# Performance work log

Measured on AMD Instinct MI355X. Metric: run time of the kernel, lower is better.

The kernel has to match this reference:

```python
import math
import jax, jax.numpy as jnp
import numpy as np

NUM_PRE_NMS = 2000
NMS_THR = 0.7
MIN_SIZE = 16.0
LOG_MAX = math.log(1000.0 / 16)  # clamp on dh, dw as in the torch module

B, A, H, W = 8, 3, 200, 304
STRIDE = 4


def _make_anchors():
    # grid anchors, channel-last anchor ordering to match permute(0,2,3,1)
    sizes = np.array([32.0, 64.0, 128.0], dtype=np.float32)  # A sizes
    ys = (np.arange(H, dtype=np.float32) + 0.5) * STRIDE
    xs = (np.arange(W, dtype=np.float32) + 0.5) * STRIDE
    cy, cx = np.meshgrid(ys, xs, indexing="ij")  # [H,W]
    cx = cx[:, :, None]
    cy = cy[:, :, None]
    half = (sizes / 2.0)[None, None, :]  # [1,1,A]
    anc = np.stack([cx - half, cy - half, cx + half, cy + half], axis=-1)  # [H,W,A,4]
    anc = anc.reshape(-1, 4)  # [H*W*A, 4]
    anc = np.broadcast_to(anc[None], (B, anc.shape[0], 4)).copy()
    return jnp.asarray(anc)


def setup_inputs() -> dict:
    key = jax.random.key(0)
    k1, k2 = jax.random.split(key)
    cls_logits = jax.random.normal(k1, (B, A, H, W), dtype=jnp.float32)
    regs = jax.random.normal(k2, (B, 4 * A, H, W), dtype=jnp.float32) * 0.1
    anchors = _make_anchors()
    return {"cls_logits": cls_logits, "regs": regs, "anchors": anchors,
            "image_h": 800, "image_w": 1216}


def _box_iou(boxes):
    # boxes: [K,4] -> iou [K,K]
    x1, y1, x2, y2 = boxes[:, 0], boxes[:, 1], boxes[:, 2], boxes[:, 3]
    area = (x2 - x1) * (y2 - y1)
    ix1 = jnp.maximum(x1[:, None], x1[None, :])
    iy1 = jnp.maximum(y1[:, None], y1[None, :])
    ix2 = jnp.minimum(x2[:, None], x2[None, :])
    iy2 = jnp.minimum(y2[:, None], y2[None, :])
    iw = jnp.clip(ix2 - ix1, 0.0)
    ih = jnp.clip(iy2 - iy1, 0.0)
    inter = iw * ih
    union = area[:, None] + area[None, :] - inter
    return inter / jnp.maximum(union, 1e-6)


def _nms_one(boxes, valid):
    # boxes sorted by descending score; greedy suppression, fixed-size keep mask
    k = boxes.shape[0]
    iou = _box_iou(boxes)
    later = jnp.arange(k)

    def body(i, keep):
        sup = (iou[i] > NMS_THR) & keep[i] & (later > i)
        return keep & ~sup

    return jax.lax.fori_loop(0, k, body, valid)


def reference(cls_logits, regs, anchors, image_h, image_w):
    b = cls_logits.shape[0]
    # scores/regs in channel-last anchor order (matches permute(0,2,3,1))
    scores = jnp.transpose(cls_logits, (0, 2, 3, 1)).reshape(b, -1)       # [B,N]
    deltas = jnp.transpose(regs, (0, 2, 3, 1)).reshape(b, -1, 4)          # [B,N,4]
    n = scores.shape[1]
    k = min(NUM_PRE_NMS, n)

    top_scores, idx = jax.lax.top_k(scores, k)                            # [B,K]
    top_deltas = jnp.take_along_axis(deltas, idx[:, :, None], axis=1)     # [B,K,4]
    top_anchors = jnp.take_along_axis(anchors, idx[:, :, None], axis=1)   # [B,K,4]

    dx, dy = top_deltas[..., 0], top_deltas[..., 1]
    dh = jnp.minimum(top_deltas[..., 2], LOG_MAX)
    dw = jnp.minimum(top_deltas[..., 3], LOG_MAX)
    ah = top_anchors[..., 3] - top_anchors[..., 1]
    aw = top_anchors[..., 2] - top_anchors[..., 0]
    cx = aw / 2
    cy = ah / 2
    px = cx + dx * aw
    py = cy + dy * ah
    ph = jnp.exp(dh) * ah
    pw = jnp.exp(dw) * aw
    boxes = jnp.stack([px - pw / 2, py - ph / 2, px + pw / 2, py + ph / 2], axis=-1)  # [B,K,4]

    # size filter on clamped coords (as in _nms)
    w_img = jnp.float32(image_w)
    h_img = jnp.float32(image_h)
    bw = jnp.clip(boxes[..., 2], 0.0, w_img) - jnp.clip(boxes[..., 0], 0.0, w_img)
    bh = jnp.clip(boxes[..., 3], 0.0, h_img) - jnp.clip(boxes[..., 1], 0.0, h_img)
    valid = (bw >= MIN_SIZE) & (bh >= MIN_SIZE)

    keep = jax.vmap(_nms_one)(boxes, valid)                               # [B,K]
    out_boxes = boxes * keep[..., None].astype(boxes.dtype)
    return out_boxes, top_scores, keep
```

## Files before the change

### kernel.cpp

```cpp
#include <hip/hip_runtime.h>

#define HWSZ 60800
#define NA 3
#define NTOT 182400
#define KSEL 2000
#define BUFCAP 2048
#define CANDCAP 8192
#define NBATCH 8
#define GSPLIT 128
#define LOG_MAX_F 4.135166556742356f

#define OFF_H1    0
#define OFF_CCNT  65536
#define ZR_BYTES  65568
#define OFF_SEL   65568
#define OFF_BOX   65696
#define OFF_VALID 321696
#define OFF_SUP   385696
#define OFF_CAND  385696

__device__ __forceinline__ unsigned int xform(float f) {
    unsigned int b = __float_as_uint(f);
    return b ^ ((unsigned int)((int)b >> 31) | 0x80000000u);
}

__global__ __launch_bounds__(256) void k_hist1(const float* __restrict__ cls,
                                               unsigned int* __restrict__ hist1) {
    int b = blockIdx.y, part = blockIdx.x, tid = threadIdx.x;
    __shared__ unsigned int h[2048];
    for (int i = tid; i < 2048; i += 256) h[i] = 0u;
    __syncthreads();
    const float4* base4 = (const float4*)(cls + (size_t)b * NTOT);
    const int n4 = NTOT / 4;
    int per = (n4 + GSPLIT - 1) / GSPLIT;
    int lo = part * per, hi = lo + per;
    if (hi > n4) hi = n4;
    for (int i = lo + tid; i < hi; i += 256) {
        float4 v = base4[i];
        atomicAdd(&h[xform(v.x) >> 21], 1u);
        atomicAdd(&h[xform(v.y) >> 21], 1u);
        atomicAdd(&h[xform(v.z) >> 21], 1u);
        atomicAdd(&h[xform(v.w) >> 21], 1u);
    }
    __syncthreads();
    unsigned int* gh = hist1 + b * 2048;
    for (int i = tid; i < 2048; i += 256)
        if (h[i]) atomicAdd(&gh[i], h[i]);
}

__global__ __launch_bounds__(1024) void k_scan1(const unsigned int* __restrict__ hist1,
                                                uint4* __restrict__ selinfo) {
    int b = blockIdx.x, tid = threadIdx.x;
    __shared__ unsigned int sa[2048], sb[2048];
    const unsigned int* h = hist1 + b * 2048;
    sa[tid] = h[tid];
    sa[tid + 1024] = h[tid + 1024];
    unsigned int* src = sa; unsigned int* dst = sb;
    for (int d = 1; d < 2048; d <<= 1) {
        __syncthreads();
        dst[tid] = src[tid] + ((tid + d < 2048) ? src[tid + d] : 0u);
        int i2 = tid + 1024;
        dst[i2] = src[i2] + ((i2 + d < 2048) ? src[i2 + d] : 0u);
        unsigned int* t = src; src = dst; dst = t;
    }
    __syncthreads();
    #pragma unroll
    for (int k = 0; k < 2; ++k) {
        int i = tid + k * 1024;
        unsigned int c = src[i];
        unsigned int cn = (i < 2047) ? src[i + 1] : 0u;
        if (c >= KSEL && cn < KSEL)
            selinfo[b] = make_uint4((unsigned int)i, cn, KSEL - cn, 0u);
    }
}

__global__ __launch_bounds__(256) void k_gather(const float* __restrict__ cls,
                                                const uint4* __restrict__ selinfo,
                                                unsigned long long* __restrict__ cand,
                                                unsigned int* __restrict__ ccnt) {
    int b = blockIdx.y, part = blockIdx.x, tid = threadIdx.x;
    unsigned int bin = selinfo[b].x;
    __shared__ unsigned long long lbuf[1024];
    __shared__ unsigned int lcnt, gbase;
    if (tid == 0) lcnt = 0u;
    __syncthreads();
    const float4* base4 = (const float4*)(cls + (size_t)b * NTOT);
    const int n4 = NTOT / 4;
    int per = (n4 + GSPLIT - 1) / GSPLIT;
    int lo = part * per, hi = lo + per;
    if (hi > n4) hi = n4;
    for (int i = lo + tid; i < hi; i += 256) {
        float4 v = base4[i];
        float vals[4] = {v.x, v.y, v.z, v.w};
        int idx0 = i * 4;
        #pragma unroll
        for (int q = 0; q < 4; ++q) {
            unsigned int u = xform(vals[q]);
            if ((u >> 21) >= bin) {
                int idx = idx0 + q;
                int a = idx / HWSZ;
                int hw = idx - a * HWSZ;
                unsigned int n = (unsigned int)(hw * NA + a);
                unsigned int pos = atomicAdd(&lcnt, 1u);
                if (pos < 1024u)
                    lbuf[pos] = ((unsigned long long)u << 32) | (unsigned long long)(~n);
            }
        }
    }
    __syncthreads();
    if (tid == 0) {
        unsigned int c = lcnt < 1024u ? lcnt : 1024u;
        gbase = atomicAdd(&ccnt[b], c);
    }
    __syncthreads();
    unsigned int c = lcnt < 1024u ? lcnt : 1024u;
    unsigned int gb = gbase;
    for (unsigned int i = tid; i < c; i += 256) {
        unsigned int p = gb + i;
        if (p < CANDCAP) cand[(size_t)b * CANDCAP + p] = lbuf[i];
    }
}

__global__ __launch_bounds__(1024) void k_sort_decode(
        const unsigned long long* __restrict__ cand,
        const unsigned int* __restrict__ ccnt,
        const uint4* __restrict__ selinfo,
        const float* __restrict__ regs,
        const float* __restrict__ anchors,
        const int* __restrict__ img_h,
        const int* __restrict__ img_w,
        float* __restrict__ out_scores,
        float4* __restrict__ boxes_ws,
        unsigned int* __restrict__ valid_ws) {
    int b = blockIdx.x;
    int tid = threadIdx.x;
    __shared__ unsigned long long arr[BUFCAP];
    __shared__ unsigned int sa[2048], sb[2048];
    __shared__ unsigned int acnt, shT;
    uint4 si = selinfo[b];
    unsigned int bin = si.x, krem = si.z;
    unsigned int m = ccnt[b];
    if (m > CANDCAP) m = CANDCAP;
    const unsigned long long* cb = cand + (size_t)b * CANDCAP;

    sa[tid] = 0u; sa[tid + 1024] = 0u;
    if (tid == 0) acnt = 0u;
    __syncthreads();
    for (unsigned int i = tid; i < m; i += 1024) {
        unsigned int u = (unsigned int)(cb[i] >> 32);
        if ((u >> 21) == bin) atomicAdd(&sa[(u >> 10) & 2047u], 1u);
    }
    unsigned int* src = sa; unsigned int* dst = sb;
    for (int d = 1; d < 2048; d <<= 1) {
        __syncthreads();
        dst[tid] = src[tid] + ((tid + d < 2048) ? src[tid + d] : 0u);
        int i2 = tid + 1024;
        dst[i2] = src[i2] + ((i2 + d < 2048) ? src[i2 + d] : 0u);
        unsigned int* t = src; src = dst; dst = t;
    }
    __syncthreads();
    #pragma unroll
    for (int k = 0; k < 2; ++k) {
        int i = tid + k * 1024;
        unsigned int c = src[i];
        unsigned int cn = (i < 2047) ? src[i + 1] : 0u;
        if (c >= krem && cn < krem)
            shT = (bin << 21) | ((unsigned int)i << 10);
    }
    __syncthreads();
    unsigned int T = shT;

    int lane = tid & 63;
    unsigned long long lmask = (1ULL << lane) - 1ULL;
    unsigned int mr = (m + 1023u) & ~1023u;
    for (unsigned int i = tid; i < mr; i += 1024) {
        bool pred = false;
        unsigned long long key = 0ULL;
        if (i < m) {
            key = cb[i];
            pred = ((unsigned int)(key >> 32)) >= T;
        }
        unsigned long long mask = __ballot(pred);
        unsigned int cw = (unsigned int)__popcll(mask);
        unsigned int base = 0u;
        if (lane == 0 && cw) base = atomicAdd(&acnt, cw);
        base = __shfl(base, 0, 64);
        if (pred) {
            unsigned int pos = base + (unsigned int)__popcll(mask & lmask);
            if (pos < BUFCAP) arr[pos] = key;
        }
    }
    __syncthreads();
    unsigned int total = acnt < BUFCAP ? acnt : BUFCAP;
    for (unsigned int i = tid; i < BUFCAP; i += 1024)
        if (i >= total) arr[i] = 0ULL;
    __syncthreads();

    for (int k = 2; k <= BUFCAP; k <<= 1) {
        for (int j = k >> 1; j > 0; j >>= 1) {
            for (int i = tid; i < BUFCAP; i += 1024) {
                int ixj = i ^ j;
                if (ixj > i) {
                    unsigned long long x = arr[i], y = arr[ixj];
                    bool up = (i & k) == 0;
                    if (up ? (x < y) : (x > y)) { arr[i] = y; arr[ixj] = x; }
                }
            }
            __syncthreads();
        }
    }

    int hv = img_h[0];
    int wv = img_w[0];
    float himg = (hv > 0 && hv < 100000) ? (float)hv : __int_as_float(hv);
    float wimg = (wv > 0 && wv < 100000) ? (float)wv : __int_as_float(wv);

    for (int r = tid; r < KSEL; r += 1024) {
        unsigned long long packed = arr[r];
        size_t o = (size_t)b * KSEL + r;
        if (packed == 0ULL) {
            out_scores[o] = 0.f;
            boxes_ws[o] = make_float4(0.f, 0.f, 0.f, 0.f);
            valid_ws[o] = 0u;
            continue;
        }
        unsigned int u = (unsigned int)(packed >> 32);
        unsigned int n = ~((unsigned int)packed);
        unsigned int bits = (u & 0x80000000u) ? (u & 0x7FFFFFFFu) : ~u;
        float score = __uint_as_float(bits);
        int a = (int)(n % NA);
        int hw = (int)(n / NA);
        const float* rp = regs + ((size_t)b * (4 * NA) + 4 * a) * HWSZ + hw;
        float dx = rp[0 * HWSZ];
        float dy = rp[1 * HWSZ];
        float dh = rp[2 * HWSZ];
        float dw = rp[3 * HWSZ];
        const float* ap = anchors + ((size_t)b * NTOT + n) * 4;
        float ax1 = ap[0], ay1 = ap[1], ax2 = ap[2], ay2 = ap[3];
        float ahh = ay2 - ay1;
        float aww = ax2 - ax1;
        float cx = aww * 0.5f;
        float cy = ahh * 0.5f;
        float px = cx + dx * aww;
        float py = cy + dy * ahh;
        dh = fminf(dh, LOG_MAX_F);
        dw = fminf(dw, LOG_MAX_F);
        float ph = expf(dh) * ahh;
        float pw = expf(dw) * aww;
        float x1 = px - pw * 0.5f;
        float y1 = py - ph * 0.5f;
        float x2 = px + pw * 0.5f;
        float y2 = py + ph * 0.5f;
        float bwv = fminf(fmaxf(x2, 0.f), wimg) - fminf(fmaxf(x1, 0.f), wimg);
        float bhv = fminf(fmaxf(y2, 0.f), himg) - fminf(fmaxf(y1, 0.f), himg);
        unsigned int valid = (bwv >= 16.f && bhv >= 16.f) ? 1u : 0u;
        out_scores[o] = score;
        boxes_ws[o] = make_float4(x1, y1, x2, y2);
        valid_ws[o] = valid;
    }
}

__global__ __launch_bounds__(256) void k_supmat(const float4* __restrict__ boxes_ws,
                                                unsigned long long* __restrict__ sup) {
    int ct = blockIdx.x;
    int rt = blockIdx.y;
    int b  = blockIdx.z;
    int tid = threadIdx.x;
    __shared__ float4 colbox[64];
    int j0 = ct * 64;
    if (tid < 64) {
        int jl = j0 + tid;
        colbox[tid] = (jl < KSEL) ? boxes_ws[(size_t)b * KSEL + jl]
                                  : make_float4(0.f, 0.f, 0.f, 0.f);
    }
    __syncthreads();
    int i = rt * 256 + tid;
    if (i >= KSEL) return;
    float4 bi = boxes_ws[(size_t)b * KSEL + i];
    float area_i = (bi.z - bi.x) * (bi.w - bi.y);
    unsigned long long word = 0ULL;
    #pragma unroll 8
    for (int jj = 0; jj < 64; ++jj) {
        int j = j0 + jj;
        float4 bj = colbox[jj];
        float area_j = (bj.z - bj.x) * (bj.w - bj.y);
        float ix1 = fmaxf(bi.x, bj.x);
        float iy1 = fmaxf(bi.y, bj.y);
        float ix2 = fminf(bi.z, bj.z);
        float iy2 = fminf(bi.w, bj.w);
        float iw = fmaxf(ix2 - ix1, 0.f);
        float ih = fmaxf(iy2 - iy1, 0.f);
        float inter = iw * ih;
        float uni = area_i + area_j - inter;
        float iou = inter / fmaxf(uni, 1e-6f);
        bool s = (j > i) && (j < KSEL) && (iou > 0.7f);
        if (s) word |= (1ULL << jj);
    }
    sup[((size_t)b * KSEL + i) * 32 + ct] = word;
}

__global__ __launch_bounds__(256) void k_nms_scan(const unsigned long long* __restrict__ sup,
                                                  const unsigned int* __restrict__ valid_ws,
                                                  const float4* __restrict__ boxes_ws,
                                                  float* __restrict__ out_boxes,
                                                  float* __restrict__ out_keep) {
    int b = blockIdx.x;
    int tid = threadIdx.x;
    int lane = tid & 63;
    int myword = tid & 31;
    __shared__ unsigned long long kws[32];
    __shared__ unsigned long long fin[32];
    __shared__ unsigned long long diag[64];
    __shared__ unsigned int accw[64];
    const unsigned long long* srow = sup + (size_t)b * KSEL * 32;

    if (tid < 32) {
        unsigned long long kw = 0ULL;
        const uint4* vv = (const uint4*)(valid_ws + (size_t)b * KSEL);
        #pragma unroll 4
        for (int q = 0; q < 16; ++q) {
            uint4 x = vv[tid * 16 + q];
            int base = q * 4;
            if (x.x) kw |= 1ULL << (base + 0);
            if (x.y) kw |= 1ULL << (base + 1);
            if (x.z) kw |= 1ULL << (base + 2);
            if (x.w) kw |= 1ULL << (base + 3);
        }
        if (tid == 31) kw &= 0xFFFFULL;
        kws[tid] = kw;
    }
    if (tid < 64) accw[tid] = 0u;

    unsigned long long curv[8], nxt[8];
    #pragma unroll
    for (int k = 0; k < 8; ++k) curv[k] = srow[tid + k * 256];

    for (int w = 0; w < 32; ++w) {
        if (myword == w) {
            #pragma unroll
            for (int k = 0; k < 8; ++k) diag[(tid >> 5) + k * 8] = curv[k];
        }
        __syncthreads();

        if (w < 31) {
            int gbase = (w + 1) * 2048;
            #pragma unroll
            for (int k = 0; k < 8; ++k) {
                int e = tid + k * 256;
                int row = (w + 1) * 64 + (e >> 5);
                nxt[k] = (row < KSEL) ? srow[gbase + e] : 0ULL;
            }
        }

        unsigned long long dval = diag[lane];
        unsigned int dlo = (unsigned int)dval;
        unsigned int dhi = (unsigned int)(dval >> 32);
        unsigned long long k0 = kws[w];
        unsigned long long pend = ((unsigned long long)accw[w * 2 + 1] << 32)
                                  | (unsigned long long)accw[w * 2];
        unsigned long long c64 = k0 & ~pend;
        unsigned int clo = __builtin_amdgcn_readfirstlane((unsigned int)c64);
        unsigned int chi = __builtin_amdgcn_readfirstlane((unsigned int)(c64 >> 32));
        unsigned long long cur = ((unsigned long long)chi << 32) | (unsigned long long)clo;
        #pragma unroll
        for (int bit = 0; bit < 64; ++bit) {
            if ((cur >> bit) & 1ULL) {
                unsigned int lo = (unsigned int)__builtin_amdgcn_readlane((int)dlo, bit);
                unsigned int hi = (unsigned int)__builtin_amdgcn_readlane((int)dhi, bit);
                cur &= ~(((unsigned long long)hi << 32) | (unsigned long long)lo);
            }
        }
        if (tid == 0) fin[w] = cur;

        unsigned long long v = 0ULL;
        #pragma unroll
        for (int k = 0; k < 8; ++k) {
            int row = (tid + k * 256) >> 5;
            if ((cur >> row) & 1ULL) v |= curv[k];
        }
        v |= __shfl_xor(v, 32, 64);
        if (lane < 32 && v) {
            atomicOr(&accw[myword * 2], (unsigned int)v);
            atomicOr(&accw[myword * 2 + 1], (unsigned int)(v >> 32));
        }

        #pragma unroll
        for (int k = 0; k < 8; ++k) curv[k] = nxt[k];
    }
    __syncthreads();

    for (int r = tid; r < KSEL; r += 256) {
        float kf = (float)((fin[r >> 6] >> (r & 63)) & 1ULL);
        size_t o = (size_t)b * KSEL + r;
        out_keep[o] = kf;
        float4 bx = boxes_ws[o];
        float* ob = out_boxes + o * 4;
        ob[0] = bx.x * kf;
        ob[1] = bx.y * kf;
        ob[2] = bx.z * kf;
        ob[3] = bx.w * kf;
    }
}

extern "C" void kernel_launch(void* const* d_in, const int* in_sizes, int n_in,
                              void* d_out, int out_size, void* d_ws, size_t ws_size,
                              hipStream_t stream) {
    const float* cls     = (const float*)d_in[0];
    const float* regs    = (const float*)d_in[1];
    const float* anchors = (const float*)d_in[2];
    const int*   img_h   = (const int*)d_in[3];
    const int*   img_w   = (const int*)d_in[4];

    float* out = (float*)d_out;
    float* out_boxes  = out;
    float* out_scores = out + 64000;
    float* out_keep   = out + 80000;

    char* ws = (char*)d_ws;
    unsigned int* hist1      = (unsigned int*)(ws + OFF_H1);
    unsigned int* ccnt       = (unsigned int*)(ws + OFF_CCNT);
    uint4* selinfo           = (uint4*)(ws + OFF_SEL);
    float4* boxes_ws         = (float4*)(ws + OFF_BOX);
    unsigned int* valid_ws   = (unsigned int*)(ws + OFF_VALID);
    unsigned long long* sup  = (unsigned long long*)(ws + OFF_SUP);
    unsigned long long* cand = (unsigned long long*)(ws + OFF_CAND);

    hipMemsetAsync(ws, 0, ZR_BYTES, stream);
    k_hist1<<<dim3(GSPLIT, NBATCH), 256, 0, stream>>>(cls, hist1);
    k_scan1<<<NBATCH, 1024, 0, stream>>>(hist1, selinfo);
    k_gather<<<dim3(GSPLIT, NBATCH), 256, 0, stream>>>(cls, selinfo, cand, ccnt);
    k_sort_decode<<<NBATCH, 1024, 0, stream>>>(cand, ccnt, selinfo, regs, anchors,
                                               img_h, img_w, out_scores, boxes_ws, valid_ws);
    k_supmat<<<dim3(32, 8, NBATCH), 256, 0, stream>>>(boxes_ws, sup);
    k_nms_scan<<<NBATCH, 256, 0, stream>>>(sup, valid_ws, boxes_ws, out_boxes, out_keep);
}
```

Baseline: 244.9 us.

## Replace single-block bitonic sort with parallel rank-by-counting across many blocks

Splits the per-batch sort-and-decode kernel in two. A refine kernel does threshold selection and writes the surviving keys to a workspace buffer. A rank-decode kernel launched over 10x8 blocks then computes each key's output position by counting larger keys, using wave readlane broadcasts, and decodes the box directly at that rank. This replaces a bitonic sort run by only 8 workgroups with many barriers, in exchange for O(n^2) comparisons, an extra launch and a global round-trip. Slots below KSEL are no longer zero-filled when fewer than KSEL candidates survive, and keys past index 2560 are never ranked.

```diff
diff --git a/kernel.cpp b/kernel.cpp
--- a/kernel.cpp
+++ b/kernel.cpp
@@ -4,20 +4,22 @@
 #define NA 3
 #define NTOT 182400
 #define KSEL 2000
-#define BUFCAP 2048
 #define CANDCAP 8192
+#define SELCAP 4096
 #define NBATCH 8
 #define GSPLIT 128
 #define LOG_MAX_F 4.135166556742356f
 
 #define OFF_H1    0
 #define OFF_CCNT  65536
-#define ZR_BYTES  65568
-#define OFF_SEL   65568
-#define OFF_BOX   65696
-#define OFF_VALID 321696
-#define OFF_SUP   385696
-#define OFF_CAND  385696
+#define OFF_SCNT  65568
+#define ZR_BYTES  65600
+#define OFF_SEL   65600
+#define OFF_BOX   65728
+#define OFF_VALID 321728
+#define OFF_SUP   385728
+#define OFF_CAND  385728
+#define OFF_SELK  910016
 
 __device__ __forceinline__ unsigned int xform(float f) {
     unsigned int b = __float_as_uint(f);
@@ -121,10 +123,76 @@
     }
 }
 
-__global__ __launch_bounds__(1024) void k_sort_decode(
-        const unsigned long long* __restrict__ cand,
-        const unsigned int* __restrict__ ccnt,
-        const uint4* __restrict__ selinfo,
+__global__ __launch_bounds__(1024) void k_refine(const unsigned long long* __restrict__ cand,
+                                                 const unsigned int* __restrict__ ccnt,
+                                                 const uint4* __restrict__ selinfo,
+                                                 unsigned long long* __restrict__ selk,
+                                                 unsigned int* __restrict__ scnt) {
+    int b = blockIdx.x;
+    int tid = threadIdx.x;
+    __shared__ unsigned int sa[2048], sb[2048];
+    __shared__ unsigned int acnt, shT;
+    uint4 si = selinfo[b];
+    unsigned int bin = si.x, krem = si.z;
+    unsigned int m = ccnt[b];
+    if (m > CANDCAP) m = CANDCAP;
+    const unsigned long long* cb = cand + (size_t)b * CANDCAP;
+
+    sa[tid] = 0u; sa[tid + 1024] = 0u;
+    if (tid == 0) acnt = 0u;
+    __syncthreads();
+    for (unsigned int i = tid; i < m; i += 1024) {
+        unsigned int u = (unsigned int)(cb[i] >> 32);
+        if ((u >> 21) == bin) atomicAdd(&sa[(u >> 10) & 2047u], 1u);
+    }
+    unsigned int* src = sa; unsigned int* dst = sb;
+    for (int d = 1; d < 2048; d <<= 1) {
+        __syncthreads();
+        dst[tid] = src[tid] + ((tid + d < 2048) ? src[tid + d] : 0u);
+        int i2 = tid + 1024;
+        dst[i2] = src[i2] + ((i2 + d < 2048) ? src[i2 + d] : 0u);
+        unsigned int* t = src; src = dst; dst = t;
+    }
+    __syncthreads();
+    #pragma unroll
+    for (int k = 0; k < 2; ++k) {
+        int i = tid + k * 1024;
+        unsigned int c = src[i];
+        unsigned int cn = (i < 2047) ? src[i + 1] : 0u;
+        if (c >= krem && cn < krem)
+            shT = (bin << 21) | ((unsigned int)i << 10);
+    }
+    __syncthreads();
+    unsigned int T = shT;
+
+    int lane = tid & 63;
+    unsigned long long lmask = (1ULL << lane) - 1ULL;
+    unsigned int mr = (m + 1023u) & ~1023u;
+    unsigned long long* sout = selk + (size_t)b * SELCAP;
+    for (unsigned int i = tid; i < mr; i += 1024) {
+        bool pred = false;
+        unsigned long long key = 0ULL;
+        if (i < m) {
+            key = cb[i];
+            pred = ((unsigned int)(key >> 32)) >= T;
+        }
+        unsigned long long mask = __ballot(pred);
+        unsigned int cw = (unsigned int)__popcll(mask);
+        unsigned int base = 0u;
+        if (lane == 0 && cw) base = atomicAdd(&acnt, cw);
+        base = __shfl(base, 0, 64);
+        if (pred) {
+            unsigned int pos = base + (unsigned int)__popcll(mask & lmask);
+            if (pos < SELCAP) sout[pos] = key;
+        }
+    }
+    __syncthreads();
+    if (tid == 0) scnt[b] = (acnt < SELCAP) ? acnt : SELCAP;
+}
+
+__global__ __launch_bounds__(256) void k_rank_decode(
+        const unsigned long long* __restrict__ selk,
+        const unsigned int* __restrict__ scnt,
         const float* __restrict__ regs,
         const float* __restrict__ anchors,
         const int* __restrict__ img_h,
@@ -132,132 +200,71 @@
         float* __restrict__ out_scores,
         float4* __restrict__ boxes_ws,
         unsigned int* __restrict__ valid_ws) {
-    int b = blockIdx.x;
+    int b = blockIdx.y;
     int tid = threadIdx.x;
-    __shared__ unsigned long long arr[BUFCAP];
-    __shared__ unsigned int sa[2048], sb[2048];
-    __shared__ unsigned int acnt, shT;
-    uint4 si = selinfo[b];
-    unsigned int bin = si.x, krem = si.z;
-    unsigned int m = ccnt[b];
-    if (m > CANDCAP) m = CANDCAP;
-    const unsigned long long* cb = cand + (size_t)b * CANDCAP;
-
-    sa[tid] = 0u; sa[tid + 1024] = 0u;
-    if (tid == 0) acnt = 0u;
-    __syncthreads();
-    for (unsigned int i = tid; i < m; i += 1024) {
-        unsigned int u = (unsigned int)(cb[i] >> 32);
-        if ((u >> 21) == bin) atomicAdd(&sa[(u >> 10) & 2047u], 1u);
-    }
-    unsigned int* src = sa; unsigned int* dst = sb;
-    for (int d = 1; d < 2048; d <<= 1) {
-        __syncthreads();
-        dst[tid] = src[tid] + ((tid + d < 2048) ? src[tid + d] : 0u);
-        int i2 = tid + 1024;
-        dst[i2] = src[i2] + ((i2 + d < 2048) ? src[i2 + d] : 0u);
-        unsigned int* t = src; src = dst; dst = t;
-    }
-    __syncthreads();
-    #pragma unroll
-    for (int k = 0; k < 2; ++k) {
-        int i = tid + k * 1024;
-        unsigned int c = src[i];
-        unsigned int cn = (i < 2047) ? src[i + 1] : 0u;
-        if (c >= krem && cn < krem)
-            shT = (bin << 21) | ((unsigned int)i << 10);
-    }
-    __syncthreads();
-    unsigned int T = shT;
-
     int lane = tid & 63;
-    unsigned long long lmask = (1ULL << lane) - 1ULL;
-    unsigned int mr = (m + 1023u) & ~1023u;
-    for (unsigned int i = tid; i < mr; i += 1024) {
-        bool pred = false;
-        unsigned long long key = 0ULL;
-        if (i < m) {
-            key = cb[i];
-            pred = ((unsigned int)(key >> 32)) >= T;
-        }
-        unsigned long long mask = __ballot(pred);
-        unsigned int cw = (unsigned int)__popcll(mask);
-        unsigned int base = 0u;
-        if (lane == 0 && cw) base = atomicAdd(&acnt, cw);
-        base = __shfl(base, 0, 64);
-        if (pred) {
-            unsigned int pos = base + (unsigned int)__popcll(mask & lmask);
-            if (pos < BUFCAP) arr[pos] = key;
-        }
-    }
-    __syncthreads();
-    unsigned int total = acnt < BUFCAP ? acnt : BUFCAP;
-    for (unsigned int i = tid; i < BUFCAP; i += 1024)
-        if (i >= total) arr[i] = 0ULL;
-    __syncthreads();
-
-    for (int k = 2; k <= BUFCAP; k <<= 1) {
-        for (int j = k >> 1; j > 0; j >>= 1) {
-            for (int i = tid; i < BUFCAP; i += 1024) {
-                int ixj = i ^ j;
-                if (ixj > i) {
-                    unsigned long long x = arr[i], y = arr[ixj];
-                    bool up = (i & k) == 0;
-                    if (up ? (x < y) : (x > y)) { arr[i] = y; arr[ixj] = x; }
-                }
-            }
-            __syncthreads();
-        }
-    }
+    unsigned int sc = scnt[b];
+    if (sc > SELCAP) sc = SELCAP;
+    unsigned int r = blockIdx.x * 256 + tid;
+    if (blockIdx.x * 256 >= sc) return;
+    const unsigned long long* sb_ = selk + (size_t)b * SELCAP;
+    unsigned long long mykey = (r < sc) ? sb_[r] : 0ULL;
+
+    unsigned int cnt = 0u;
+    for (unsigned int base = 0; base < sc; base += 64) {
+        unsigned long long kj = 0ULL;
+        if (base + (unsigned int)lane < sc) kj = sb_[base + lane];
+        unsigned int klo = (unsigned int)kj;
+        unsigned int khi = (unsigned int)(kj >> 32);
+        #pragma unroll
+        for (int t = 0; t < 64; ++t) {
+            unsigned int lo = (unsigned int)__builtin_amdgcn_readlane((int)klo, t);
+            unsigned int hi = (unsigned int)__builtin_amdgcn_readlane((int)khi, t);
+            unsigned long long kt = ((unsigned long long)hi << 32) | (unsigned long long)lo;
+            cnt += (kt > mykey) ? 1u : 0u;
+        }
+    }
+    if (r >= sc || cnt >= KSEL) return;
 
     int hv = img_h[0];
     int wv = img_w[0];
     float himg = (hv > 0 && hv < 100000) ? (float)hv : __int_as_float(hv);
     float wimg = (wv > 0 && wv < 100000) ? (float)wv : __int_as_float(wv);
 
-    for (int r = tid; r < KSEL; r += 1024) {
-        unsigned long long packed = arr[r];
-        size_t o = (size_t)b * KSEL + r;
-        if (packed == 0ULL) {
-            out_scores[o] = 0.f;
-            boxes_ws[o] = make_float4(0.f, 0.f, 0.f, 0.f);
-            valid_ws[o] = 0u;
-            continue;
-        }
-        unsigned int u = (unsigned int)(packed >> 32);
-        unsigned int n = ~((unsigned int)packed);
-        unsigned int bits = (u & 0x80000000u) ? (u & 0x7FFFFFFFu) : ~u;
-        float score = __uint_as_float(bits);
-        int a = (int)(n % NA);
-        int hw = (int)(n / NA);
-        const float* rp = regs + ((size_t)b * (4 * NA) + 4 * a) * HWSZ + hw;
-        float dx = rp[0 * HWSZ];
-        float dy = rp[1 * HWSZ];
-        float dh = rp[2 * HWSZ];
-        float dw = rp[3 * HWSZ];
-        const float* ap = anchors + ((size_t)b * NTOT + n) * 4;
-        float ax1 = ap[0], ay1 = ap[1], ax2 = ap[2], ay2 = ap[3];
-        float ahh = ay2 - ay1;
-        float aww = ax2 - ax1;
-        float cx = aww * 0.5f;
-        float cy = ahh * 0.5f;
-        float px = cx + dx * aww;
-        float py = cy + dy * ahh;
-        dh = fminf(dh, LOG_MAX_F);
-        dw = fminf(dw, LOG_MAX_F);
-        float ph = expf(dh) * ahh;
-        float pw = expf(dw) * aww;
-        float x1 = px - pw * 0.5f;
-        float y1 = py - ph * 0.5f;
-        float x2 = px + pw * 0.5f;
-        float y2 = py + ph * 0.5f;
-        float bwv = fminf(fmaxf(x2, 0.f), wimg) - fminf(fmaxf(x1, 0.f), wimg);
-        float bhv = fminf(fmaxf(y2, 0.f), himg) - fminf(fmaxf(y1, 0.f), himg);
-        unsigned int valid = (bwv >= 16.f && bhv >= 16.f) ? 1u : 0u;
-        out_scores[o] = score;
-        boxes_ws[o] = make_float4(x1, y1, x2, y2);
-        valid_ws[o] = valid;
-    }
+    unsigned int u = (unsigned int)(mykey >> 32);
+    unsigned int n = ~((unsigned int)mykey);
+    unsigned int bits = (u & 0x80000000u) ? (u & 0x7FFFFFFFu) : ~u;
+    float score = __uint_as_float(bits);
+    int a = (int)(n % NA);
+    int hw = (int)(n / NA);
+    const float* rp = regs + ((size_t)b * (4 * NA) + 4 * a) * HWSZ + hw;
+    float dx = rp[0 * HWSZ];
+    float dy = rp[1 * HWSZ];
+    float dh = rp[2 * HWSZ];
+    float dw = rp[3 * HWSZ];
+    const float* ap = anchors + ((size_t)b * NTOT + n) * 4;
+    float ax1 = ap[0], ay1 = ap[1], ax2 = ap[2], ay2 = ap[3];
+    float ahh = ay2 - ay1;
+    float aww = ax2 - ax1;
+    float cx = aww * 0.5f;
+    float cy = ahh * 0.5f;
+    float px = cx + dx * aww;
+    float py = cy + dy * ahh;
+    dh = fminf(dh, LOG_MAX_F);
+    dw = fminf(dw, LOG_MAX_F);
+    float ph = expf(dh) * ahh;
+    float pw = expf(dw) * aww;
+    float x1 = px - pw * 0.5f;
+    float y1 = py - ph * 0.5f;
+    float x2 = px + pw * 0.5f;
+    float y2 = py + ph * 0.5f;
+    float bwv = fminf(fmaxf(x2, 0.f), wimg) - fminf(fmaxf(x1, 0.f), wimg);
+    float bhv = fminf(fmaxf(y2, 0.f), himg) - fminf(fmaxf(y1, 0.f), himg);
+    unsigned int valid = (bwv >= 16.f && bhv >= 16.f) ? 1u : 0u;
+    size_t o = (size_t)b * KSEL + cnt;
+    out_scores[o] = score;
+    boxes_ws[o] = make_float4(x1, y1, x2, y2);
+    valid_ws[o] = valid;
 }
 
 __global__ __launch_bounds__(256) void k_supmat(const float4* __restrict__ boxes_ws,
@@ -419,18 +426,22 @@
     char* ws = (char*)d_ws;
     unsigned int* hist1      = (unsigned int*)(ws + OFF_H1);
     unsigned int* ccnt       = (unsigned int*)(ws + OFF_CCNT);
+    unsigned int* scnt       = (unsigned int*)(ws + OFF_SCNT);
     uint4* selinfo           = (uint4*)(ws + OFF_SEL);
     float4* boxes_ws         = (float4*)(ws + OFF_BOX);
     unsigned int* valid_ws   = (unsigned int*)(ws + OFF_VALID);
     unsigned long long* sup  = (unsigned long long*)(ws + OFF_SUP);
     unsigned long long* cand = (unsigned long long*)(ws + OFF_CAND);
+    unsigned long long* selk = (unsigned long long*)(ws + OFF_SELK);
 
     hipMemsetAsync(ws, 0, ZR_BYTES, stream);
     k_hist1<<<dim3(GSPLIT, NBATCH), 256, 0, stream>>>(cls, hist1);
     k_scan1<<<NBATCH, 1024, 0, stream>>>(hist1, selinfo);
     k_gather<<<dim3(GSPLIT, NBATCH), 256, 0, stream>>>(cls, selinfo, cand, ccnt);
-    k_sort_decode<<<NBATCH, 1024, 0, stream>>>(cand, ccnt, selinfo, regs, anchors,
-                                               img_h, img_w, out_scores, boxes_ws, valid_ws);
+    k_refine<<<NBATCH, 1024, 0, stream>>>(cand, ccnt, selinfo, selk, scnt);
+    k_rank_decode<<<dim3(10, NBATCH), 256, 0, stream>>>(selk, scnt, regs, anchors,
+                                                        img_h, img_w, out_scores,
+                                                        boxes_ws, valid_ws);
     k_supmat<<<dim3(32, 8, NBATCH), 256, 0, stream>>>(boxes_ws, sup);
     k_nms_scan<<<NBATCH, 256, 0, stream>>>(sup, valid_ws, boxes_ws, out_boxes, out_keep);
 }
```

Result: faster. 231.9 us (-5.3%).
